# Optimization experiments

Measured on AMD Instinct MI355X. Metric: run time of the kernel, lower is better.

Reference implementation:

```python
import jax, jax.numpy as jnp
import numpy as np

B, N, KD, VD, ID, H = 2, 2048, 1024, 1024, 1024, 16
HD = ID // H
SCALE = ID ** (-0.5)  # module quirk: scale uses inner_dim, not head_dim
EPS = 1e-5


def layernorm(x, g, b):
    mu = jnp.mean(x, axis=-1, keepdims=True)
    var = jnp.var(x, axis=-1, keepdims=True)
    return (x - mu) * jax.lax.rsqrt(var + EPS) * g + b


def setup_inputs() -> dict:
    key = jax.random.key(0)
    ks = jax.random.split(key, 12)
    d = {
        "keys": jax.random.normal(ks[0], (B, N, KD), jnp.float32),
        "values": jax.random.normal(ks[1], (B, N, VD), jnp.float32),
        "qk_norm_g": jnp.ones((KD,), jnp.float32),
        "qk_norm_b": jnp.zeros((KD,), jnp.float32),
        "value_norm_g": jnp.ones((VD,), jnp.float32),
        "value_norm_b": jnp.zeros((VD,), jnp.float32),
        "key_norm_g": jnp.ones((ID,), jnp.float32),
        "key_norm_b": jnp.zeros((ID,), jnp.float32),
        "query_norm_g": jnp.ones((ID,), jnp.float32),
        "query_norm_b": jnp.zeros((ID,), jnp.float32),
        "w_qk": jax.random.normal(ks[2], (KD, 2 * ID), jnp.float32) * (KD ** -0.5),
        "w_v": jax.random.normal(ks[3], (VD, ID), jnp.float32) * (VD ** -0.5),
        "w_out": jax.random.normal(ks[4], (ID, VD), jnp.float32) * (ID ** -0.5),
        "b_out": jnp.zeros((VD,), jnp.float32),
    }
    return d


def reference(keys, values, qk_norm_g, qk_norm_b, value_norm_g, value_norm_b,
              key_norm_g, key_norm_b, query_norm_g, query_norm_b,
              w_qk, w_v, w_out, b_out):
    keys = layernorm(keys, qk_norm_g, qk_norm_b)
    values = layernorm(values, value_norm_g, value_norm_b)
    qk = keys @ w_qk  # [B,N,2*ID]
    q, k = qk[..., :ID], qk[..., ID:]
    q = layernorm(q, query_norm_g, query_norm_b)
    k = layernorm(k, key_norm_g, key_norm_b)
    # b n (h d) -> b h n d
    q = q.reshape(B, N, H, HD).transpose(0, 2, 1, 3)
    k = k.reshape(B, N, H, HD).transpose(0, 2, 1, 3)
    v = (values @ w_v).reshape(B, N, H, HD).transpose(0, 2, 1, 3)
    dots = jnp.einsum('bhqd,bhkd->bhqk', q, k) * SCALE
    attn = jax.nn.softmax(dots, axis=-1)
    out = jnp.einsum('bhqk,bhkd->bhqd', attn, v)
    out = out.transpose(0, 2, 1, 3).reshape(B, N, ID)
    return out @ w_out + b_out
```

## Files before the change

### kernel.cpp

```cpp
#include <hip/hip_runtime.h>
#include <hip/hip_bf16.h>
#include <type_traits>


typedef __hip_bfloat16 bf16;
typedef __attribute__((ext_vector_type(8))) short bf16x8;
typedef __attribute__((ext_vector_type(4))) float f32x4;

#define MFMA_BF16(a, b, c) __builtin_amdgcn_mfma_f32_16x16x32_bf16((a), (b), (c), 0, 0, 0)

__device__ __forceinline__ float us2f(unsigned short u) {
  unsigned int v = ((unsigned int)u) << 16;
  return __builtin_bit_cast(float, v);
}

__device__ __forceinline__ unsigned pack_bf16x2(float a, float b) {
  union { __hip_bfloat162 h; unsigned u; } cv;
  cv.h = __float22bfloat162_rn(float2{a, b});
  return cv.u;
}

__device__ __forceinline__ unsigned pack_bf16x2_trunc(float a, float b) {
  return __builtin_amdgcn_perm(__builtin_bit_cast(unsigned, b),
                               __builtin_bit_cast(unsigned, a), 0x07060302u);
}

__device__ __forceinline__ void gl_lds16(const bf16* g, bf16* l) {
  __builtin_amdgcn_global_load_lds(
      (const __attribute__((address_space(1))) void*)g,
      (__attribute__((address_space(3))) void*)l, 16, 0, 0);
}

template <typename TIN>
__global__ __launch_bounds__(256) void ln2_kernel(
    const TIN* __restrict__ in0, const TIN* __restrict__ in1, int stride,
    const float* __restrict__ g0, const float* __restrict__ b0,
    const float* __restrict__ g1, const float* __restrict__ b1,
    bf16* __restrict__ out0, bf16* __restrict__ out1, int D,
    float sc0, float sc1)
{
  const int which = blockIdx.y;
  const TIN* in = which ? in1 : in0;
  const float* gamma = which ? g1 : g0;
  const float* beta = which ? b1 : b0;
  bf16* out = which ? out1 : out0;
  const float sc = which ? sc1 : sc0;
  const int row = blockIdx.x;
  const int t = threadIdx.x;
  float x0, x1, x2, x3;
  if constexpr (std::is_same_v<TIN, float>) {
    float4 u = *(const float4*)(in + (size_t)row * stride + t * 4);
    x0 = u.x; x1 = u.y; x2 = u.z; x3 = u.w;
  } else {
    ushort4 u = *(const ushort4*)(in + (size_t)row * stride + t * 4);
    x0 = us2f(u.x); x1 = us2f(u.y); x2 = us2f(u.z); x3 = us2f(u.w);
  }
  float s = x0 + x1 + x2 + x3;
  float s2 = x0 * x0 + x1 * x1 + x2 * x2 + x3 * x3;
#pragma unroll
  for (int m = 1; m < 64; m <<= 1) {
    s += __shfl_xor(s, m);
    s2 += __shfl_xor(s2, m);
  }
  __shared__ float red[10];
  const int w = t >> 6, lane = t & 63;
  if (lane == 0) { red[w] = s; red[4 + w] = s2; }
  __syncthreads();
  if (t == 0) {
    float S = red[0] + red[1] + red[2] + red[3];
    float S2 = red[4] + red[5] + red[6] + red[7];
    float mu = S / (float)D;
    float var = S2 / (float)D - mu * mu;
    red[8] = mu;
    red[9] = rsqrtf(var + 1e-5f);
  }
  __syncthreads();
  const float mu = red[8], rs = red[9];
  float4 g4 = *(const float4*)(gamma + t * 4);
  float4 b4 = *(const float4*)(beta + t * 4);
  uint2 o;
  o.x = pack_bf16x2(((x0 - mu) * rs * g4.x + b4.x) * sc, ((x1 - mu) * rs * g4.y + b4.y) * sc);
  o.y = pack_bf16x2(((x2 - mu) * rs * g4.z + b4.z) * sc, ((x3 - mu) * rs * g4.w + b4.w) * sc);
  *(uint2*)(out + (size_t)row * D + t * 4) = o;
}

__global__ __launch_bounds__(256) void transpose_kernel(
    const float* __restrict__ s0, bf16* __restrict__ d0,
    const float* __restrict__ s1, bf16* __restrict__ d1, int R, int C)
{
  __shared__ float tile[64][68];
  const float* in = (s1 && blockIdx.z) ? s1 : s0;
  bf16* out = (s1 && blockIdx.z) ? d1 : d0;
  const int r0 = blockIdx.y * 64, c0 = blockIdx.x * 64;
  const int t = threadIdx.x;
  const int lr = t >> 2, lc = (t & 3) * 16;
  const float* src = in + (size_t)(r0 + lr) * C + (c0 + lc);
#pragma unroll
  for (int i = 0; i < 4; ++i) {
    float4 u = *(const float4*)(src + i * 4);
    tile[lr][lc + i * 4 + 0] = u.x;
    tile[lr][lc + i * 4 + 1] = u.y;
    tile[lr][lc + i * 4 + 2] = u.z;
    tile[lr][lc + i * 4 + 3] = u.w;
  }
  __syncthreads();
  __align__(16) bf16 tmp[16];
#pragma unroll
  for (int j = 0; j < 16; ++j) tmp[j] = __float2bfloat16(tile[lc + j][lr]);
  bf16* dst = out + (size_t)(c0 + lr) * R + (r0 + lc);
  *(bf16x8*)dst       = *(const bf16x8*)&tmp[0];
  *(bf16x8*)(dst + 8) = *(const bf16x8*)&tmp[8];
}

template <int BM, int TMODE, typename TOUT>
__global__ __launch_bounds__(256) void gemm_bt_kernel(
    const bf16* __restrict__ A, const bf16* __restrict__ Bt,
    const float* __restrict__ bias, TOUT* __restrict__ C,
    int M, int N, int K, int has_bias)
{
  constexpr int MT = BM / 32;
  constexpr int LA = (BM * 4) / 256;
  __shared__ __align__(16) bf16 lA[2 * BM * 32];
  __shared__ __align__(16) bf16 lB[2 * 128 * 32];
  const int t = threadIdx.x;
  const int w = t >> 6, lane = t & 63, l15 = lane & 15, quad = lane >> 4;
  const int wy = w >> 1, wx = w & 1;
  const bf16* Ab = A + (size_t)blockIdx.y * BM * K;
  const bf16* Bb = Bt + (size_t)blockIdx.x * 128 * K;
  f32x4 acc[MT][4] = {};

#pragma unroll
  for (int i = 0; i < LA; ++i) {
    int s = i * 256 + t;
    gl_lds16(Ab + (size_t)(s >> 2) * K + (s & 3) * 8, lA + s * 8);
  }
#pragma unroll
  for (int i = 0; i < 2; ++i) {
    int s = i * 256 + t;
    gl_lds16(Bb + (size_t)(s >> 2) * K + (s & 3) * 8, lB + s * 8);
  }

  const int niter = K >> 5;
  for (int it = 0; it < niter; ++it) {
    const int cur = it & 1;
    __builtin_amdgcn_s_barrier();
    {
      int nkc = (it + 1 < niter) ? (it + 1) * 32 : 0;
      bf16* dA = lA + (cur ^ 1) * BM * 32;
      bf16* dB = lB + (cur ^ 1) * 4096;
#pragma unroll
      for (int i = 0; i < LA; ++i) {
        int s = i * 256 + t;
        gl_lds16(Ab + (size_t)(s >> 2) * K + nkc + (s & 3) * 8, dA + s * 8);
      }
#pragma unroll
      for (int i = 0; i < 2; ++i) {
        int s = i * 256 + t;
        gl_lds16(Bb + (size_t)(s >> 2) * K + nkc + (s & 3) * 8, dB + s * 8);
      }
    }
    if constexpr (LA + 2 == 4) asm volatile("s_waitcnt vmcnt(4)" ::: "memory");
    else                       asm volatile("s_waitcnt vmcnt(3)" ::: "memory");
    __builtin_amdgcn_s_barrier();

    const bf16* sA = lA + cur * BM * 32;
    const bf16* sB = lB + cur * 4096;
    bf16x8 af[MT], bfr[4];
#pragma unroll
    for (int mt = 0; mt < MT; ++mt)
      af[mt] = *(const bf16x8*)&sA[(wy * (BM / 2) + mt * 16 + l15) * 32 + quad * 8];
#pragma unroll
    for (int nt = 0; nt < 4; ++nt)
      bfr[nt] = *(const bf16x8*)&sB[(wx * 64 + nt * 16 + l15) * 32 + quad * 8];
#pragma unroll
    for (int mt = 0; mt < MT; ++mt)
#pragma unroll
      for (int nt = 0; nt < 4; ++nt)
        acc[mt][nt] = MFMA_BF16(af[mt], bfr[nt], acc[mt][nt]);
  }

  const int row_base = blockIdx.y * BM + wy * (BM / 2);
  const int col_base = blockIdx.x * 128 + wx * 64;
#pragma unroll
  for (int mt = 0; mt < MT; ++mt)
#pragma unroll
    for (int nt = 0; nt < 4; ++nt) {
      const int col = col_base + nt * 16 + l15;
      if constexpr (TMODE == 1) {
        const int row0 = row_base + mt * 16 + quad * 4;
        const int b = row0 >> 11, n0 = row0 & 2047;
        uint2 ok;
        ok.x = pack_bf16x2(acc[mt][nt][0], acc[mt][nt][1]);
        ok.y = pack_bf16x2(acc[mt][nt][2], acc[mt][nt][3]);
        *(uint2*)&((bf16*)C)[((size_t)(b << 10) + col) * 2048 + n0] = ok;
      } else {
        const float bb = has_bias ? bias[col] : 0.0f;
#pragma unroll
        for (int r = 0; r < 4; ++r) {
          const int row = row_base + mt * 16 + quad * 4 + r;
          float v = acc[mt][nt][r] + bb;
          if constexpr (std::is_same_v<TOUT, bf16>)
            C[(size_t)row * N + col] = __float2bfloat16(v);
          else
            C[(size_t)row * N + col] = v;
        }
      }
    }
}

__global__ __launch_bounds__(256) void flash_kernel(
    const bf16* __restrict__ Q, const bf16* __restrict__ Km,
    const bf16* __restrict__ Vt, bf16* __restrict__ O)
{
  __shared__ __align__(16) bf16 smem[9216 + 8192 + 8192 + 8192];
  bf16* lP = smem;
  bf16* lQ = smem + 9216;
  bf16* lKb = smem + 9216 + 8192;
  bf16* lVb = smem + 9216 + 8192 + 8192;
  const int t = threadIdx.x;
  const int w = t >> 6, lane = t & 63, l15 = lane & 15, quad = lane >> 4;
  const int qt = blockIdx.x, bh = blockIdx.y;
  const int b = bh >> 4, h = bh & 15;
  const int qrow0 = b * 2048 + qt * 128;
  const bf16* qbase = Q + (size_t)qrow0 * 1024 + h * 64;
  const bf16* kbase = Km + ((size_t)(b * 2048)) * 1024 + h * 64;
  const bf16* vbase = Vt + ((size_t)(b * 1024 + h * 64)) * 2048;
  bf16* lPm = lP + w * (32 * 72);

  const int sr0 = t >> 3, sc0 = ((t & 7) ^ (sr0 & 7)) << 3;
  const int sr1 = (256 + t) >> 3, sc1 = (((256 + t) & 7) ^ (sr1 & 7)) << 3;
  const bf16* kp0 = kbase + sr0 * 1024 + sc0;
  const bf16* kp1 = kbase + sr1 * 1024 + sc1;
  const bf16* vp0 = vbase + sr0 * 2048 + sc0;
  const bf16* vp1 = vbase + sr1 * 2048 + sc1;

#pragma unroll
  for (int i = 0; i < 4; ++i) {
    int s = i * 256 + t;
    int row = s >> 3, c = (s & 7) ^ (row & 7);
    gl_lds16(qbase + (size_t)row * 1024 + (c << 3), lQ + s * 8);
  }
  gl_lds16(kp0, lKb + t * 8);
  gl_lds16(kp1, lKb + (256 + t) * 8);
  gl_lds16(vp0, lVb + t * 8);
  gl_lds16(vp1, lVb + (256 + t) * 8);
  asm volatile("s_waitcnt vmcnt(4)" ::: "memory");
  __builtin_amdgcn_s_barrier();

  const int sw = (quad ^ (l15 & 7)) << 3;
  bf16x8 qf[2][2];
#pragma unroll
  for (int mset = 0; mset < 2; ++mset) {
    const int row = w * 32 + mset * 16 + l15;
    qf[mset][0] = *(const bf16x8*)&lQ[row * 64 + sw];
    qf[mset][1] = *(const bf16x8*)&lQ[row * 64 + (sw ^ 32)];
  }

  f32x4 o_acc[4][2] = {};
  f32x4 l_vec[2] = {};

  for (int kt = 0; kt < 32; ++kt) {
    const int cur = kt & 1;
    bf16* lK = lKb + cur * 4096;
    bf16* lV = lVb + cur * 4096;
    bf16* lKn = lKb + (cur ^ 1) * 4096;
    bf16* lVn = lVb + (cur ^ 1) * 4096;

    __builtin_amdgcn_s_barrier();
    {
      const int ktn = (kt + 1) & 31;
      const int ko = ktn << 16;
      const int vo = ktn << 6;
      gl_lds16(kp0 + ko, lKn + t * 8);
      gl_lds16(kp1 + ko, lKn + (256 + t) * 8);
      gl_lds16(vp0 + vo, lVn + t * 8);
      gl_lds16(vp1 + vo, lVn + (256 + t) * 8);
    }
    asm volatile("s_waitcnt vmcnt(4)" ::: "memory");
    __builtin_amdgcn_s_barrier();

    bf16x8 kf[4][2];
#pragma unroll
    for (int nt = 0; nt < 4; ++nt) {
      kf[nt][0] = *(const bf16x8*)&lK[(nt * 16 + l15) * 64 + sw];
      kf[nt][1] = *(const bf16x8*)&lK[(nt * 16 + l15) * 64 + (sw ^ 32)];
    }

#pragma unroll
    for (int mset = 0; mset < 2; ++mset) {
#pragma unroll
      for (int nt = 0; nt < 4; ++nt) {
        f32x4 z = {};
        z = MFMA_BF16(kf[nt][0], qf[mset][0], z);
        z = MFMA_BF16(kf[nt][1], qf[mset][1], z);
        f32x4 p;
#pragma unroll
        for (int r = 0; r < 4; ++r) p[r] = __builtin_amdgcn_exp2f(z[r]);
        l_vec[mset] += p;
        uint2 pk;
        pk.x = pack_bf16x2_trunc(p[0], p[1]);
        pk.y = pack_bf16x2_trunc(p[2], p[3]);
        *(uint2*)&lPm[(mset * 16 + l15) * 72 + nt * 16 + quad * 4] = pk;
      }
    }

    bf16x8 vf[4][2];
#pragma unroll
    for (int dt = 0; dt < 4; ++dt) {
      vf[dt][0] = *(const bf16x8*)&lV[(dt * 16 + l15) * 64 + sw];
      vf[dt][1] = *(const bf16x8*)&lV[(dt * 16 + l15) * 64 + (sw ^ 32)];
    }
    asm volatile("s_waitcnt lgkmcnt(0)" ::: "memory");

#pragma unroll
    for (int mset = 0; mset < 2; ++mset) {
      const bf16* pr = &lPm[(mset * 16 + l15) * 72 + quad * 8];
      bf16x8 pf0 = *(const bf16x8*)pr;
      bf16x8 pf1 = *(const bf16x8*)(pr + 32);
#pragma unroll
      for (int dt = 0; dt < 4; ++dt) {
        o_acc[dt][mset] = MFMA_BF16(vf[dt][0], pf0, o_acc[dt][mset]);
        o_acc[dt][mset] = MFMA_BF16(vf[dt][1], pf1, o_acc[dt][mset]);
      }
    }
  }

#pragma unroll
  for (int mset = 0; mset < 2; ++mset) {
    float tsum = l_vec[mset][0] + l_vec[mset][1] + l_vec[mset][2] + l_vec[mset][3];
    tsum += __shfl_xor(tsum, 16);
    tsum += __shfl_xor(tsum, 32);
    const float inv = 1.0f / tsum;
    const int m = qrow0 + w * 32 + mset * 16 + l15;
#pragma unroll
    for (int dt = 0; dt < 4; ++dt) {
      uint2 ok;
      ok.x = pack_bf16x2(o_acc[dt][mset][0] * inv, o_acc[dt][mset][1] * inv);
      ok.y = pack_bf16x2(o_acc[dt][mset][2] * inv, o_acc[dt][mset][3] * inv);
      *(uint2*)&O[(size_t)m * 1024 + h * 64 + dt * 16 + quad * 4] = ok;
    }
  }
}

extern "C" void kernel_launch(void* const* d_in, const int* in_sizes, int n_in,
                              void* d_out, int out_size, void* d_ws, size_t ws_size,
                              hipStream_t stream)
{
  (void)in_sizes; (void)n_in; (void)out_size; (void)ws_size;
  const float* keys   = (const float*)d_in[0];
  const float* values = (const float*)d_in[1];
  const float* qk_g   = (const float*)d_in[2];
  const float* qk_b   = (const float*)d_in[3];
  const float* val_g  = (const float*)d_in[4];
  const float* val_b  = (const float*)d_in[5];
  const float* key_g  = (const float*)d_in[6];
  const float* key_b  = (const float*)d_in[7];
  const float* qry_g  = (const float*)d_in[8];
  const float* qry_b  = (const float*)d_in[9];
  const float* w_qk   = (const float*)d_in[10];
  const float* w_v    = (const float*)d_in[11];
  const float* w_out  = (const float*)d_in[12];
  const float* b_out  = (const float*)d_in[13];
  float* out = (float*)d_out;

  const float CEXP = 0.03125f * 1.44269504f;

  char* ws = (char*)d_ws;
  const size_t MB = 1024 * 1024;
  bf16* keys_ln   = (bf16*)(ws + 0);
  bf16* values_ln = (bf16*)(ws + 8 * MB);
  bf16* qk        = (bf16*)(ws + 16 * MB);
  bf16* attn      = (bf16*)(ws + 16 * MB);
  bf16* vt        = (bf16*)(ws + 24 * MB);
  bf16* qln       = (bf16*)(ws + 32 * MB);
  bf16* kln       = (bf16*)(ws + 40 * MB);
  bf16* wqkT      = (bf16*)(ws + 48 * MB);
  bf16* wvT       = (bf16*)(ws + 52 * MB);
  bf16* woutT     = (bf16*)(ws + 54 * MB);

  ln2_kernel<float><<<dim3(4096, 2), 256, 0, stream>>>(
      keys, values, 1024, qk_g, qk_b, val_g, val_b, keys_ln, values_ln, 1024, 1.0f, 1.0f);
  transpose_kernel<<<dim3(32, 16, 1), 256, 0, stream>>>(w_qk, wqkT, nullptr, nullptr, 1024, 2048);
  transpose_kernel<<<dim3(16, 16, 2), 256, 0, stream>>>(w_v, wvT, w_out, woutT, 1024, 1024);
  gemm_bt_kernel<128, 0, bf16><<<dim3(16, 32), 256, 0, stream>>>(keys_ln, wqkT, nullptr, qk, 4096, 2048, 1024, 0);
  ln2_kernel<bf16><<<dim3(4096, 2), 256, 0, stream>>>(
      qk, qk + 1024, 2048, qry_g, qry_b, key_g, key_b, qln, kln, 1024, CEXP, 1.0f);
  gemm_bt_kernel<64, 1, bf16><<<dim3(8, 64), 256, 0, stream>>>(values_ln, wvT, nullptr, vt, 4096, 1024, 1024, 0);
  flash_kernel<<<dim3(16, 32), 256, 0, stream>>>(qln, kln, vt, attn);
  gemm_bt_kernel<64, 0, float><<<dim3(8, 64), 256, 0, stream>>>(attn, woutT, b_out, out, 4096, 1024, 1024, 1);
}
```

Baseline: 260.7 us.

## Merge weight transposes, stage V-GEMM transposed output in LDS, load V directly

Merges the two weight-transpose launches into a single three-slice launch whose early-exit blocks cover the smaller matrices. The transposed-output V projection GEMM now stages its tile in LDS and writes 16-byte coalesced rows instead of scattered 8-byte stores. The flash kernel drops LDS double-buffering for V and loads V fragments straight from global memory into registers at the start of each iteration, using vmcnt waits so they overlap the QK^T and softmax work. This saves LDS and launch overhead, but V reads now come from global or cache per wave instead of being shared through LDS.

```diff
diff --git a/kernel.cpp b/kernel.cpp
--- a/kernel.cpp
+++ b/kernel.cpp
@@ -84,13 +84,17 @@
   *(uint2*)(out + (size_t)row * D + t * 4) = o;
 }
 
-__global__ __launch_bounds__(256) void transpose_kernel(
+__global__ __launch_bounds__(256) void transpose3_kernel(
     const float* __restrict__ s0, bf16* __restrict__ d0,
-    const float* __restrict__ s1, bf16* __restrict__ d1, int R, int C)
+    const float* __restrict__ s1, bf16* __restrict__ d1,
+    const float* __restrict__ s2, bf16* __restrict__ d2)
 {
+  const int z = blockIdx.z;
+  if (z > 0 && blockIdx.x >= 16) return;
+  const float* in = (z == 0) ? s0 : (z == 1) ? s1 : s2;
+  bf16* out = (z == 0) ? d0 : (z == 1) ? d1 : d2;
+  const int R = 1024, C = (z == 0) ? 2048 : 1024;
   __shared__ float tile[64][68];
-  const float* in = (s1 && blockIdx.z) ? s1 : s0;
-  bf16* out = (s1 && blockIdx.z) ? d1 : d0;
   const int r0 = blockIdx.y * 64, c0 = blockIdx.x * 64;
   const int t = threadIdx.x;
   const int lr = t >> 2, lc = (t & 3) * 16;
@@ -122,6 +126,8 @@
   constexpr int LA = (BM * 4) / 256;
   __shared__ __align__(16) bf16 lA[2 * BM * 32];
   __shared__ __align__(16) bf16 lB[2 * 128 * 32];
+  constexpr int OUTSZ = (TMODE == 1) ? 128 * 68 : 1;
+  __shared__ __align__(16) bf16 lOut[OUTSZ];
   const int t = threadIdx.x;
   const int w = t >> 6, lane = t & 63, l15 = lane & 15, quad = lane >> 4;
   const int wy = w >> 1, wx = w & 1;
@@ -179,21 +185,41 @@
         acc[mt][nt] = MFMA_BF16(af[mt], bfr[nt], acc[mt][nt]);
   }
 
-  const int row_base = blockIdx.y * BM + wy * (BM / 2);
-  const int col_base = blockIdx.x * 128 + wx * 64;
-#pragma unroll
-  for (int mt = 0; mt < MT; ++mt)
-#pragma unroll
-    for (int nt = 0; nt < 4; ++nt) {
-      const int col = col_base + nt * 16 + l15;
-      if constexpr (TMODE == 1) {
-        const int row0 = row_base + mt * 16 + quad * 4;
-        const int b = row0 >> 11, n0 = row0 & 2047;
-        uint2 ok;
-        ok.x = pack_bf16x2(acc[mt][nt][0], acc[mt][nt][1]);
-        ok.y = pack_bf16x2(acc[mt][nt][2], acc[mt][nt][3]);
-        *(uint2*)&((bf16*)C)[((size_t)(b << 10) + col) * 2048 + n0] = ok;
-      } else {
+  if constexpr (TMODE == 1) {
+    __syncthreads();
+#pragma unroll
+    for (int mt = 0; mt < MT; ++mt)
+#pragma unroll
+      for (int nt = 0; nt < 4; ++nt) {
+        const int d = wx * 64 + nt * 16 + l15;
+        const int n = wy * 32 + mt * 16 + quad * 4;
+        uint2 pk;
+        pk.x = pack_bf16x2(acc[mt][nt][0], acc[mt][nt][1]);
+        pk.y = pack_bf16x2(acc[mt][nt][2], acc[mt][nt][3]);
+        *(uint2*)&lOut[d * 68 + n] = pk;
+      }
+    __syncthreads();
+    const int row0 = blockIdx.y * BM;
+    const int bidx = row0 >> 11, n0 = row0 & 2047;
+    const int col0 = blockIdx.x * 128;
+    const int d = t >> 1, half = (t & 1) * 32;
+    const bf16* src = &lOut[d * 68 + half];
+    __align__(16) bf16 tmp[32];
+#pragma unroll
+    for (int j = 0; j < 8; ++j)
+      *(uint2*)&tmp[j * 4] = *(const uint2*)(src + j * 4);
+    bf16* g = (bf16*)C + ((size_t)(bidx << 10) + col0 + d) * 2048 + n0 + half;
+#pragma unroll
+    for (int j = 0; j < 4; ++j)
+      *(bf16x8*)(g + j * 8) = *(const bf16x8*)&tmp[j * 8];
+  } else {
+    const int row_base = blockIdx.y * BM + wy * (BM / 2);
+    const int col_base = blockIdx.x * 128 + wx * 64;
+#pragma unroll
+    for (int mt = 0; mt < MT; ++mt)
+#pragma unroll
+      for (int nt = 0; nt < 4; ++nt) {
+        const int col = col_base + nt * 16 + l15;
         const float bb = has_bias ? bias[col] : 0.0f;
 #pragma unroll
         for (int r = 0; r < 4; ++r) {
@@ -205,18 +231,17 @@
             C[(size_t)row * N + col] = v;
         }
       }
-    }
+  }
 }
 
 __global__ __launch_bounds__(256) void flash_kernel(
     const bf16* __restrict__ Q, const bf16* __restrict__ Km,
     const bf16* __restrict__ Vt, bf16* __restrict__ O)
 {
-  __shared__ __align__(16) bf16 smem[9216 + 8192 + 8192 + 8192];
+  __shared__ __align__(16) bf16 smem[9216 + 8192 + 8192];
   bf16* lP = smem;
   bf16* lQ = smem + 9216;
   bf16* lKb = smem + 9216 + 8192;
-  bf16* lVb = smem + 9216 + 8192 + 8192;
   const int t = threadIdx.x;
   const int w = t >> 6, lane = t & 63, l15 = lane & 15, quad = lane >> 4;
   const int qt = blockIdx.x, bh = blockIdx.y;
@@ -231,8 +256,7 @@
   const int sr1 = (256 + t) >> 3, sc1 = (((256 + t) & 7) ^ (sr1 & 7)) << 3;
   const bf16* kp0 = kbase + sr0 * 1024 + sc0;
   const bf16* kp1 = kbase + sr1 * 1024 + sc1;
-  const bf16* vp0 = vbase + sr0 * 2048 + sc0;
-  const bf16* vp1 = vbase + sr1 * 2048 + sc1;
+  const bf16* vlane = vbase + l15 * 2048 + quad * 8;
 
 #pragma unroll
   for (int i = 0; i < 4; ++i) {
@@ -242,9 +266,7 @@
   }
   gl_lds16(kp0, lKb + t * 8);
   gl_lds16(kp1, lKb + (256 + t) * 8);
-  gl_lds16(vp0, lVb + t * 8);
-  gl_lds16(vp1, lVb + (256 + t) * 8);
-  asm volatile("s_waitcnt vmcnt(4)" ::: "memory");
+  asm volatile("s_waitcnt vmcnt(2)" ::: "memory");
   __builtin_amdgcn_s_barrier();
 
   const int sw = (quad ^ (l15 & 7)) << 3;
@@ -262,21 +284,24 @@
   for (int kt = 0; kt < 32; ++kt) {
     const int cur = kt & 1;
     bf16* lK = lKb + cur * 4096;
-    bf16* lV = lVb + cur * 4096;
     bf16* lKn = lKb + (cur ^ 1) * 4096;
-    bf16* lVn = lVb + (cur ^ 1) * 4096;
 
     __builtin_amdgcn_s_barrier();
+
+    bf16x8 vf[4][2];
+#pragma unroll
+    for (int dt = 0; dt < 4; ++dt) {
+      const bf16* vp = vlane + dt * (16 * 2048) + kt * 64;
+      vf[dt][0] = *(const bf16x8*)vp;
+      vf[dt][1] = *(const bf16x8*)(vp + 32);
+    }
     {
       const int ktn = (kt + 1) & 31;
       const int ko = ktn << 16;
-      const int vo = ktn << 6;
       gl_lds16(kp0 + ko, lKn + t * 8);
       gl_lds16(kp1 + ko, lKn + (256 + t) * 8);
-      gl_lds16(vp0 + vo, lVn + t * 8);
-      gl_lds16(vp1 + vo, lVn + (256 + t) * 8);
-    }
-    asm volatile("s_waitcnt vmcnt(4)" ::: "memory");
+    }
+    asm volatile("s_waitcnt vmcnt(10)" ::: "memory");
     __builtin_amdgcn_s_barrier();
 
     bf16x8 kf[4][2];
@@ -303,14 +328,8 @@
         *(uint2*)&lPm[(mset * 16 + l15) * 72 + nt * 16 + quad * 4] = pk;
       }
     }
-
-    bf16x8 vf[4][2];
-#pragma unroll
-    for (int dt = 0; dt < 4; ++dt) {
-      vf[dt][0] = *(const bf16x8*)&lV[(dt * 16 + l15) * 64 + sw];
-      vf[dt][1] = *(const bf16x8*)&lV[(dt * 16 + l15) * 64 + (sw ^ 32)];
-    }
     asm volatile("s_waitcnt lgkmcnt(0)" ::: "memory");
+    asm volatile("s_waitcnt vmcnt(2)" ::: "memory");
 
 #pragma unroll
     for (int mset = 0; mset < 2; ++mset) {
@@ -380,8 +399,7 @@
 
   ln2_kernel<float><<<dim3(4096, 2), 256, 0, stream>>>(
       keys, values, 1024, qk_g, qk_b, val_g, val_b, keys_ln, values_ln, 1024, 1.0f, 1.0f);
-  transpose_kernel<<<dim3(32, 16, 1), 256, 0, stream>>>(w_qk, wqkT, nullptr, nullptr, 1024, 2048);
-  transpose_kernel<<<dim3(16, 16, 2), 256, 0, stream>>>(w_v, wvT, w_out, woutT, 1024, 1024);
+  transpose3_kernel<<<dim3(32, 16, 3), 256, 0, stream>>>(w_qk, wqkT, w_v, wvT, w_out, woutT);
   gemm_bt_kernel<128, 0, bf16><<<dim3(16, 32), 256, 0, stream>>>(keys_ln, wqkT, nullptr, qk, 4096, 2048, 1024, 0);
   ln2_kernel<bf16><<<dim3(4096, 2), 256, 0, stream>>>(
       qk, qk + 1024, 2048, qry_g, qry_b, key_g, key_b, qln, kln, 1024, CEXP, 1.0f);
```

Measured after the change: 269.8 us. +3.5%, slower.

## Merge weight transposes, shrink GEMM tiles, stage transposed V output through LDS

Applied to the files above, without the earlier changes.

Folds the two weight-transpose launches into one three-slice launch. The GEMM kernel gets a BN template parameter, and the three GEMMs use smaller tiles (64x128, 64x64) to launch more blocks. The double-buffered prefetch pipeline is removed in favour of a simple load-sync-compute loop. The transposed V output is now written through an LDS tile so global stores are coalesced 16-byte writes. Losing the software pipelining may expose global load latency, and smaller tiles lower per-block data reuse.

```diff
diff --git a/kernel.cpp b/kernel.cpp
--- a/kernel.cpp
+++ b/kernel.cpp
@@ -84,13 +84,17 @@
   *(uint2*)(out + (size_t)row * D + t * 4) = o;
 }
 
-__global__ __launch_bounds__(256) void transpose_kernel(
+__global__ __launch_bounds__(256) void transpose3_kernel(
     const float* __restrict__ s0, bf16* __restrict__ d0,
-    const float* __restrict__ s1, bf16* __restrict__ d1, int R, int C)
-{
+    const float* __restrict__ s1, bf16* __restrict__ d1,
+    const float* __restrict__ s2, bf16* __restrict__ d2)
+{
+  const int z = blockIdx.z;
+  if (z > 0 && blockIdx.x >= 16) return;
+  const float* in = (z == 0) ? s0 : (z == 1) ? s1 : s2;
+  bf16* out = (z == 0) ? d0 : (z == 1) ? d1 : d2;
+  const int R = 1024, C = (z == 0) ? 2048 : 1024;
   __shared__ float tile[64][68];
-  const float* in = (s1 && blockIdx.z) ? s1 : s0;
-  bf16* out = (s1 && blockIdx.z) ? d1 : d0;
   const int r0 = blockIdx.y * 64, c0 = blockIdx.x * 64;
   const int t = threadIdx.x;
   const int lr = t >> 2, lc = (t & 3) * 16;
@@ -112,88 +116,85 @@
   *(bf16x8*)(dst + 8) = *(const bf16x8*)&tmp[8];
 }
 
-template <int BM, int TMODE, typename TOUT>
+template <int BM, int BN, int TMODE, typename TOUT>
 __global__ __launch_bounds__(256) void gemm_bt_kernel(
     const bf16* __restrict__ A, const bf16* __restrict__ Bt,
     const float* __restrict__ bias, TOUT* __restrict__ C,
     int M, int N, int K, int has_bias)
 {
-  constexpr int MT = BM / 32;
-  constexpr int LA = (BM * 4) / 256;
-  __shared__ __align__(16) bf16 lA[2 * BM * 32];
-  __shared__ __align__(16) bf16 lB[2 * 128 * 32];
+  constexpr int MT = BM / 32, NT = BN / 32;
+  constexpr int ASL = (BM * 4) / 256, BSL = (BN * 4) / 256;
+  __shared__ __align__(16) bf16 lA[BM * 32];
+  __shared__ __align__(16) bf16 lB[BN * 32];
+  constexpr int OUTSZ = (TMODE == 1) ? 64 * 68 : 1;
+  __shared__ __align__(16) bf16 lOut[OUTSZ];
   const int t = threadIdx.x;
   const int w = t >> 6, lane = t & 63, l15 = lane & 15, quad = lane >> 4;
   const int wy = w >> 1, wx = w & 1;
   const bf16* Ab = A + (size_t)blockIdx.y * BM * K;
-  const bf16* Bb = Bt + (size_t)blockIdx.x * 128 * K;
-  f32x4 acc[MT][4] = {};
-
-#pragma unroll
-  for (int i = 0; i < LA; ++i) {
-    int s = i * 256 + t;
-    gl_lds16(Ab + (size_t)(s >> 2) * K + (s & 3) * 8, lA + s * 8);
-  }
-#pragma unroll
-  for (int i = 0; i < 2; ++i) {
-    int s = i * 256 + t;
-    gl_lds16(Bb + (size_t)(s >> 2) * K + (s & 3) * 8, lB + s * 8);
-  }
-
-  const int niter = K >> 5;
-  for (int it = 0; it < niter; ++it) {
-    const int cur = it & 1;
-    __builtin_amdgcn_s_barrier();
-    {
-      int nkc = (it + 1 < niter) ? (it + 1) * 32 : 0;
-      bf16* dA = lA + (cur ^ 1) * BM * 32;
-      bf16* dB = lB + (cur ^ 1) * 4096;
-#pragma unroll
-      for (int i = 0; i < LA; ++i) {
-        int s = i * 256 + t;
-        gl_lds16(Ab + (size_t)(s >> 2) * K + nkc + (s & 3) * 8, dA + s * 8);
+  const bf16* Bb = Bt + (size_t)blockIdx.x * BN * K;
+  f32x4 acc[MT][NT] = {};
+
+  for (int kc = 0; kc < K; kc += 32) {
+    __syncthreads();
+#pragma unroll
+    for (int i = 0; i < ASL; ++i) {
+      int s = i * 256 + t;
+      gl_lds16(Ab + (size_t)(s >> 2) * K + kc + (s & 3) * 8, lA + s * 8);
+    }
+#pragma unroll
+    for (int i = 0; i < BSL; ++i) {
+      int s = i * 256 + t;
+      gl_lds16(Bb + (size_t)(s >> 2) * K + kc + (s & 3) * 8, lB + s * 8);
+    }
+    __syncthreads();
+    bf16x8 af[MT], bfr[NT];
+#pragma unroll
+    for (int mt = 0; mt < MT; ++mt)
+      af[mt] = *(const bf16x8*)&lA[(wy * (BM / 2) + mt * 16 + l15) * 32 + quad * 8];
+#pragma unroll
+    for (int nt = 0; nt < NT; ++nt)
+      bfr[nt] = *(const bf16x8*)&lB[(wx * (BN / 2) + nt * 16 + l15) * 32 + quad * 8];
+#pragma unroll
+    for (int mt = 0; mt < MT; ++mt)
+#pragma unroll
+      for (int nt = 0; nt < NT; ++nt)
+        acc[mt][nt] = MFMA_BF16(af[mt], bfr[nt], acc[mt][nt]);
+  }
+
+  if constexpr (TMODE == 1) {
+    __syncthreads();
+#pragma unroll
+    for (int mt = 0; mt < MT; ++mt)
+#pragma unroll
+      for (int nt = 0; nt < NT; ++nt) {
+        const int d = wx * 32 + nt * 16 + l15;
+        const int n = wy * 32 + mt * 16 + quad * 4;
+        uint2 pk;
+        pk.x = pack_bf16x2(acc[mt][nt][0], acc[mt][nt][1]);
+        pk.y = pack_bf16x2(acc[mt][nt][2], acc[mt][nt][3]);
+        *(uint2*)&lOut[d * 68 + n] = pk;
       }
-#pragma unroll
-      for (int i = 0; i < 2; ++i) {
-        int s = i * 256 + t;
-        gl_lds16(Bb + (size_t)(s >> 2) * K + nkc + (s & 3) * 8, dB + s * 8);
-      }
-    }
-    if constexpr (LA + 2 == 4) asm volatile("s_waitcnt vmcnt(4)" ::: "memory");
-    else                       asm volatile("s_waitcnt vmcnt(3)" ::: "memory");
-    __builtin_amdgcn_s_barrier();
-
-    const bf16* sA = lA + cur * BM * 32;
-    const bf16* sB = lB + cur * 4096;
-    bf16x8 af[MT], bfr[4];
+    __syncthreads();
+    const int row0 = blockIdx.y * BM;
+    const int bidx = row0 >> 11, n0 = row0 & 2047;
+    const int col0 = blockIdx.x * BN;
+    const int d = t >> 2, nh = (t & 3) * 16;
+    __align__(16) bf16 tmp[16];
+#pragma unroll
+    for (int j = 0; j < 4; ++j)
+      *(uint2*)&tmp[j * 4] = *(const uint2*)&lOut[d * 68 + nh + j * 4];
+    bf16* g = (bf16*)C + ((size_t)(bidx << 10) + col0 + d) * 2048 + n0 + nh;
+    *(bf16x8*)g       = *(const bf16x8*)&tmp[0];
+    *(bf16x8*)(g + 8) = *(const bf16x8*)&tmp[8];
+  } else {
+    const int row_base = blockIdx.y * BM + wy * (BM / 2);
+    const int col_base = blockIdx.x * BN + wx * (BN / 2);
 #pragma unroll
     for (int mt = 0; mt < MT; ++mt)
-      af[mt] = *(const bf16x8*)&sA[(wy * (BM / 2) + mt * 16 + l15) * 32 + quad * 8];
-#pragma unroll
-    for (int nt = 0; nt < 4; ++nt)
-      bfr[nt] = *(const bf16x8*)&sB[(wx * 64 + nt * 16 + l15) * 32 + quad * 8];
-#pragma unroll
-    for (int mt = 0; mt < MT; ++mt)
-#pragma unroll
-      for (int nt = 0; nt < 4; ++nt)
-        acc[mt][nt] = MFMA_BF16(af[mt], bfr[nt], acc[mt][nt]);
-  }
-
-  const int row_base = blockIdx.y * BM + wy * (BM / 2);
-  const int col_base = blockIdx.x * 128 + wx * 64;
-#pragma unroll
-  for (int mt = 0; mt < MT; ++mt)
-#pragma unroll
-    for (int nt = 0; nt < 4; ++nt) {
-      const int col = col_base + nt * 16 + l15;
-      if constexpr (TMODE == 1) {
-        const int row0 = row_base + mt * 16 + quad * 4;
-        const int b = row0 >> 11, n0 = row0 & 2047;
-        uint2 ok;
-        ok.x = pack_bf16x2(acc[mt][nt][0], acc[mt][nt][1]);
-        ok.y = pack_bf16x2(acc[mt][nt][2], acc[mt][nt][3]);
-        *(uint2*)&((bf16*)C)[((size_t)(b << 10) + col) * 2048 + n0] = ok;
-      } else {
+#pragma unroll
+      for (int nt = 0; nt < NT; ++nt) {
+        const int col = col_base + nt * 16 + l15;
         const float bb = has_bias ? bias[col] : 0.0f;
 #pragma unroll
         for (int r = 0; r < 4; ++r) {
@@ -205,7 +206,7 @@
             C[(size_t)row * N + col] = v;
         }
       }
-    }
+  }
 }
 
 __global__ __launch_bounds__(256) void flash_kernel(
@@ -380,12 +381,11 @@
 
   ln2_kernel<float><<<dim3(4096, 2), 256, 0, stream>>>(
       keys, values, 1024, qk_g, qk_b, val_g, val_b, keys_ln, values_ln, 1024, 1.0f, 1.0f);
-  transpose_kernel<<<dim3(32, 16, 1), 256, 0, stream>>>(w_qk, wqkT, nullptr, nullptr, 1024, 2048);
-  transpose_kernel<<<dim3(16, 16, 2), 256, 0, stream>>>(w_v, wvT, w_out, woutT, 1024, 1024);
-  gemm_bt_kernel<128, 0, bf16><<<dim3(16, 32), 256, 0, stream>>>(keys_ln, wqkT, nullptr, qk, 4096, 2048, 1024, 0);
+  transpose3_kernel<<<dim3(32, 16, 3), 256, 0, stream>>>(w_qk, wqkT, w_v, wvT, w_out, woutT);
+  gemm_bt_kernel<64, 128, 0, bf16><<<dim3(16, 64), 256, 0, stream>>>(keys_ln, wqkT, nullptr, qk, 4096, 2048, 1024, 0);
   ln2_kernel<bf16><<<dim3(4096, 2), 256, 0, stream>>>(
       qk, qk + 1024, 2048, qry_g, qry_b, key_g, key_b, qln, kln, 1024, CEXP, 1.0f);
-  gemm_bt_kernel<64, 1, bf16><<<dim3(8, 64), 256, 0, stream>>>(values_ln, wvT, nullptr, vt, 4096, 1024, 1024, 0);
+  gemm_bt_kernel<64, 64, 1, bf16><<<dim3(16, 64), 256, 0, stream>>>(values_ln, wvT, nullptr, vt, 4096, 1024, 1024, 0);
   flash_kernel<<<dim3(16, 32), 256, 0, stream>>>(qln, kln, vt, attn);
-  gemm_bt_kernel<64, 0, float><<<dim3(8, 64), 256, 0, stream>>>(attn, woutT, b_out, out, 4096, 1024, 1024, 1);
-}
+  gemm_bt_kernel<64, 64, 0, float><<<dim3(16, 64), 256, 0, stream>>>(attn, woutT, b_out, out, 4096, 1024, 1024, 1);
+}
```

Result: no change. 256.1 us (-1.8%).
